# Optimization experiments

Measured on AMD Instinct MI355X. Metric: run time of the kernel, lower is better.

Reference implementation:

```python
import jax, jax.numpy as jnp
import numpy as np

N_NODES = 100000
N_EDGES = 1600000
D = 128
N_GRAPHS = 128
N_LAYERS = 3


def setup_inputs() -> dict:
    key = jax.random.key(0)
    ks = jax.random.split(key, 3 + 4 * N_LAYERS)
    x = jax.random.normal(ks[0], (N_NODES, D), dtype=jnp.float32)
    edge_index = jax.random.randint(ks[1], (2, N_EDGES), 0, N_NODES, dtype=jnp.int64)
    batch = jnp.sort(jax.random.randint(ks[2], (N_NODES,), 0, N_GRAPHS, dtype=jnp.int64))
    inp = {"x": x, "edge_index": edge_index, "batch": batch}
    scale = 1.0 / np.sqrt(D)
    for l in range(N_LAYERS):
        inp[f"W1_{l}"] = jax.random.normal(ks[3 + 4 * l], (D, D), dtype=jnp.float32) * scale
        inp[f"b1_{l}"] = jnp.zeros((D,), dtype=jnp.float32)
        inp[f"W2_{l}"] = jax.random.normal(ks[4 + 4 * l], (D, D), dtype=jnp.float32) * scale
        inp[f"b2_{l}"] = jnp.zeros((D,), dtype=jnp.float32)
    return inp


def _gin_conv(x, edge_index, W1, b1, W2, b2):
    # GINConv with eps=0: out = MLP(x + sum_{j in N(i)} x_j)
    msgs = x[edge_index[0]]                                   # [E, D] gather
    agg = jax.ops.segment_sum(msgs, edge_index[1], num_segments=N_NODES)
    h = x + agg
    h = jax.nn.relu(h @ W1 + b1)
    return h @ W2 + b2


def reference(x, edge_index, batch,
              W1_0, b1_0, W2_0, b2_0,
              W1_1, b1_1, W2_1, b2_1,
              W1_2, b1_2, W2_2, b2_2):
    params = [(W1_0, b1_0, W2_0, b2_0), (W1_1, b1_1, W2_1, b2_1), (W1_2, b1_2, W2_2, b2_2)]
    h = x
    for l in range(N_LAYERS - 1):
        h = _gin_conv(h, edge_index, *params[l])
        h = jax.nn.relu(h)  # act; dropout with drop_ratio=0 is identity
    node_emb = _gin_conv(h, edge_index, *params[-1])  # JK='last'
    # global_mean_pool
    sums = jax.ops.segment_sum(node_emb, batch, num_segments=N_GRAPHS)
    counts = jax.ops.segment_sum(jnp.ones((N_NODES, 1), node_emb.dtype), batch, num_segments=N_GRAPHS)
    graph_emb = sums / jnp.maximum(counts, 1.0)
    return graph_emb
```

## Files before the change

kernel.cpp:

```cpp
#include <hip/hip_runtime.h>
#include <hip/hip_bf16.h>

#define N_NODES 100000
#define N_PAD   100032
#define N_EDGES 1600000
#define DIM 128
#define N_GRAPHS 128
#define NBKT 98
#define BSTRIDE 18432
#define TILES (N_PAD / 16)
#define GRID_MLP 1024
#define POOL_BLKS ((N_NODES + 127) / 128)
#define B1_BATCH 4096
#define B1_GRID ((N_EDGES + B1_BATCH - 1) / B1_BATCH)

typedef unsigned short u16;
typedef unsigned int u32;
typedef __attribute__((ext_vector_type(8))) short bf16x8;
typedef __attribute__((ext_vector_type(4))) float f32x4;

#define MFMA(A, B, C) __builtin_amdgcn_mfma_f32_16x16x32_bf16(A, B, C, 0, 0, 0)

__device__ __forceinline__ u16 f2bf(float x) {
    u32 u = __float_as_uint(x);
    u = (u + 0x7FFFu + ((u >> 16) & 1u)) >> 16;
    return (u16)u;
}
__device__ __forceinline__ float bf2f(u16 u) {
    return __uint_as_float(((u32)u) << 16);
}

__global__ __launch_bounds__(256) void bucket1_kernel(const int* __restrict__ src,
                                                      const int* __restrict__ dst,
                                                      u32* __restrict__ cursorB,
                                                      u32* __restrict__ pairs) {
    __shared__ int lh[NBKT];
    __shared__ u32 lbase[NBKT];
    int t = threadIdx.x;
    if (t < NBKT) lh[t] = 0;
    __syncthreads();
    int e0 = blockIdx.x * B1_BATCH;
    int d[16], s[16], rk[16];
#pragma unroll
    for (int k = 0; k < 16; ++k) {
        int e = e0 + t + k * 256;
        if (e < N_EDGES) {
            d[k] = dst[e];
            s[k] = src[e];
            rk[k] = atomicAdd(&lh[d[k] >> 10], 1);
        }
    }
    __syncthreads();
    if (t < NBKT) lbase[t] = atomicAdd(&cursorB[t], (u32)lh[t]) + (u32)(t * BSTRIDE);
    __syncthreads();
#pragma unroll
    for (int k = 0; k < 16; ++k) {
        int e = e0 + t + k * 256;
        if (e < N_EDGES) {
            u32 pos = lbase[d[k] >> 10] + (u32)rk[k];
            pairs[pos] = ((u32)(d[k] & 1023) << 22) | (u32)s[k];
        }
    }
}

__global__ __launch_bounds__(1024) void bucket2_kernel(const u32* __restrict__ cursorB,
                                                       const u32* __restrict__ pairs,
                                                       int* __restrict__ row_ptr,
                                                       int* __restrict__ csr) {
    __shared__ int lh[1024];
    __shared__ int rc[1024];
    __shared__ int bs[128];
    int b = blockIdx.x, t = threadIdx.x;

    if (t < 128) bs[t] = (t < NBKT) ? (int)cursorB[t] : 0;
    __syncthreads();
    for (int off = 1; off < 128; off <<= 1) {
        int v = (t < 128 && t >= off) ? bs[t - off] : 0;
        __syncthreads();
        if (t < 128) bs[t] += v;
        __syncthreads();
    }
    int cnt = (int)cursorB[b];
    int bbase = (b == 0) ? 0 : bs[b - 1];

    lh[t] = 0;
    __syncthreads();
    const u32* pb = pairs + (size_t)b * BSTRIDE;
    for (int i = t; i < cnt; i += 1024) atomicAdd(&lh[__builtin_nontemporal_load(pb + i) >> 22], 1);
    __syncthreads();

    int own = lh[t];
    for (int off = 1; off < 1024; off <<= 1) {
        int v = (t >= off) ? lh[t - off] : 0;
        __syncthreads();
        lh[t] += v;
        __syncthreads();
    }
    int excl = lh[t] - own;
    int node = b * 1024 + t;
    if (node < N_NODES) row_ptr[node] = bbase + excl;
    if (b == 0 && t == 0) row_ptr[N_NODES] = N_EDGES;
    rc[t] = bbase + excl;
    __syncthreads();

    for (int i = t; i < cnt; i += 1024) {
        u32 p = __builtin_nontemporal_load(pb + i);
        int pos = atomicAdd(&rc[p >> 22], 1);
        csr[pos] = (int)(p & 0x3FFFFFu);
    }
}

__global__ __launch_bounds__(256) void xprep_kernel(const float* __restrict__ x,
                                                    u16* __restrict__ hb) {
    int i = blockIdx.x * 256 + threadIdx.x;
    if (i < N_NODES * 32) {
        float4 v = ((const float4*)x)[i];
        ushort4 o;
        o.x = f2bf(v.x); o.y = f2bf(v.y); o.z = f2bf(v.z); o.w = f2bf(v.w);
        ((ushort4*)hb)[i] = o;
    }
}

__global__ __launch_bounds__(256) void agg_kernel(const u16* __restrict__ hb,
                                                  const int* __restrict__ rp,
                                                  const int* __restrict__ csr,
                                                  u16* __restrict__ Ah) {
    int node = (blockIdx.x * 256 + threadIdx.x) >> 5;
    int l = threadIdx.x & 31;
    if (node >= N_NODES) return;
    const ushort4* h4 = (const ushort4*)hb;
    ushort4 sv = h4[(size_t)node * 32 + l];
    float a0 = bf2f(sv.x), a1 = bf2f(sv.y), a2 = bf2f(sv.z), a3 = bf2f(sv.w);
    int s = rp[node], e = rp[node + 1];
    int i = s;
    for (; i + 8 <= e; i += 8) {
        ushort4 v0 = h4[(size_t)csr[i + 0] * 32 + l];
        ushort4 v1 = h4[(size_t)csr[i + 1] * 32 + l];
        ushort4 v2 = h4[(size_t)csr[i + 2] * 32 + l];
        ushort4 v3 = h4[(size_t)csr[i + 3] * 32 + l];
        ushort4 v4 = h4[(size_t)csr[i + 4] * 32 + l];
        ushort4 v5 = h4[(size_t)csr[i + 5] * 32 + l];
        ushort4 v6 = h4[(size_t)csr[i + 6] * 32 + l];
        ushort4 v7 = h4[(size_t)csr[i + 7] * 32 + l];
        a0 += ((bf2f(v0.x) + bf2f(v1.x)) + (bf2f(v2.x) + bf2f(v3.x))) +
              ((bf2f(v4.x) + bf2f(v5.x)) + (bf2f(v6.x) + bf2f(v7.x)));
        a1 += ((bf2f(v0.y) + bf2f(v1.y)) + (bf2f(v2.y) + bf2f(v3.y))) +
              ((bf2f(v4.y) + bf2f(v5.y)) + (bf2f(v6.y) + bf2f(v7.y)));
        a2 += ((bf2f(v0.z) + bf2f(v1.z)) + (bf2f(v2.z) + bf2f(v3.z))) +
              ((bf2f(v4.z) + bf2f(v5.z)) + (bf2f(v6.z) + bf2f(v7.z)));
        a3 += ((bf2f(v0.w) + bf2f(v1.w)) + (bf2f(v2.w) + bf2f(v3.w))) +
              ((bf2f(v4.w) + bf2f(v5.w)) + (bf2f(v6.w) + bf2f(v7.w)));
    }
    for (; i < e; ++i) {
        ushort4 v = h4[(size_t)csr[i] * 32 + l];
        a0 += bf2f(v.x); a1 += bf2f(v.y); a2 += bf2f(v.z); a3 += bf2f(v.w);
    }
    ushort4 hv;
    hv.x = f2bf(a0); hv.y = f2bf(a1); hv.z = f2bf(a2); hv.w = f2bf(a3);
    *(ushort4*)(Ah + (size_t)node * 128 + l * 4) = hv;
}

struct WPrepArgs {
    const float* w[6];
    u16* buf[6];
};
__global__ __launch_bounds__(256) void wprep_kernel(WPrepArgs p) {
    int m = blockIdx.y;
    int idx = blockIdx.x * 256 + threadIdx.x;
    int n = idx >> 7, k = idx & 127;
    float v = p.w[m][k * 128 + n];
    u16 hi = f2bf(v);
    p.buf[m][idx] = hi;
    p.buf[m][idx + 16384] = f2bf(v - bf2f(hi));
}

#define HS 136
__global__ __launch_bounds__(256, 2) void fused_mlp(const u16* __restrict__ Ah,
                                                    const u16* __restrict__ W1,
                                                    const float* __restrict__ b1,
                                                    const u16* __restrict__ W2,
                                                    const float* __restrict__ b2,
                                                    float* __restrict__ Cf,
                                                    u16* __restrict__ Cb, int mode) {
    __shared__ u16 Hh[64 * HS];
    __shared__ u16 Hl[64 * HS];
    int tid = threadIdx.x;
    int lane = tid & 63, wave = tid >> 6;
    int m16 = lane & 15, quad = lane >> 4;
    int colBase = wave * 32;

    float b1v[2][4], b2v[2][4];
#pragma unroll
    for (int nt = 0; nt < 2; ++nt)
#pragma unroll
        for (int rg = 0; rg < 4; ++rg) {
            int col = colBase + nt * 16 + quad * 4 + rg;
            b1v[nt][rg] = b1[col];
            b2v[nt][rg] = b2[col];
        }

    f32x4 z = {0.f, 0.f, 0.f, 0.f};
    bf16x8 aH[4][4];

    int t0 = blockIdx.x * 4;
    if (t0 < TILES) {
#pragma unroll
        for (int p = 0; p < 4; ++p) {
            const u16* ah = Ah + (size_t)((t0 + p) * 16 + m16) * 128 + quad * 8;
#pragma unroll
            for (int kb = 0; kb < 4; ++kb)
                aH[p][kb] = *(const bf16x8*)(ah + kb * 32);
        }
    }

    for (; t0 < TILES; t0 += 4 * GRID_MLP) {
        bf16x8 W1H[2][4], W1L[2][4];
#pragma unroll
        for (int nt = 0; nt < 2; ++nt) {
            int n = colBase + nt * 16 + m16;
#pragma unroll
            for (int kb = 0; kb < 4; ++kb) {
                int off = n * 128 + kb * 32 + quad * 8;
                W1H[nt][kb] = *(const bf16x8*)(W1 + off);
                W1L[nt][kb] = *(const bf16x8*)(W1 + off + 16384);
            }
        }

        f32x4 acc[4][2];
#pragma unroll
        for (int p = 0; p < 4; ++p) { acc[p][0] = z; acc[p][1] = z; }

#pragma unroll
        for (int kb = 0; kb < 4; ++kb) {
#pragma unroll
            for (int p = 0; p < 4; ++p) {
                acc[p][0] = MFMA(W1H[0][kb], aH[p][kb], acc[p][0]);
                acc[p][1] = MFMA(W1H[1][kb], aH[p][kb], acc[p][1]);
                acc[p][0] = MFMA(W1L[0][kb], aH[p][kb], acc[p][0]);
                acc[p][1] = MFMA(W1L[1][kb], aH[p][kb], acc[p][1]);
            }
        }

        __syncthreads();

#pragma unroll
        for (int p = 0; p < 4; ++p) {
#pragma unroll
            for (int nt = 0; nt < 2; ++nt) {
                ushort4 hv, lv;
#pragma unroll
                for (int rg = 0; rg < 4; ++rg) {
                    float v = fmaxf(acc[p][nt][rg] + b1v[nt][rg], 0.f);
                    u16 hi = f2bf(v);
                    ((u16*)&hv)[rg] = hi;
                    ((u16*)&lv)[rg] = f2bf(v - bf2f(hi));
                }
                int off = (p * 16 + m16) * HS + colBase + nt * 16 + quad * 4;
                *(ushort4*)&Hh[off] = hv;
                *(ushort4*)&Hl[off] = lv;
            }
        }
        __syncthreads();

        int nt0 = t0 + 4 * GRID_MLP;
        if (nt0 < TILES) {
#pragma unroll
            for (int p = 0; p < 4; ++p) {
                const u16* ah = Ah + (size_t)((nt0 + p) * 16 + m16) * 128 + quad * 8;
#pragma unroll
                for (int kb = 0; kb < 4; ++kb)
                    aH[p][kb] = *(const bf16x8*)(ah + kb * 32);
            }
        }

        bf16x8 W2H[2][4], W2L[2][4];
#pragma unroll
        for (int nt = 0; nt < 2; ++nt) {
            int n = colBase + nt * 16 + m16;
#pragma unroll
            for (int kb = 0; kb < 4; ++kb) {
                int off = n * 128 + kb * 32 + quad * 8;
                W2H[nt][kb] = *(const bf16x8*)(W2 + off);
                W2L[nt][kb] = *(const bf16x8*)(W2 + off + 16384);
            }
        }

        f32x4 acc2[4][2];
#pragma unroll
        for (int p = 0; p < 4; ++p) { acc2[p][0] = z; acc2[p][1] = z; }
#pragma unroll
        for (int kb = 0; kb < 4; ++kb) {
#pragma unroll
            for (int p = 0; p < 4; ++p) {
                int off = (p * 16 + m16) * HS + kb * 32 + quad * 8;
                bf16x8 hH = *(const bf16x8*)(&Hh[off]);
                bf16x8 hL = *(const bf16x8*)(&Hl[off]);
                acc2[p][0] = MFMA(W2H[0][kb], hH, acc2[p][0]);
                acc2[p][1] = MFMA(W2H[1][kb], hH, acc2[p][1]);
                acc2[p][0] = MFMA(W2H[0][kb], hL, acc2[p][0]);
                acc2[p][1] = MFMA(W2H[1][kb], hL, acc2[p][1]);
                acc2[p][0] = MFMA(W2L[0][kb], hH, acc2[p][0]);
                acc2[p][1] = MFMA(W2L[1][kb], hH, acc2[p][1]);
            }
        }

#pragma unroll
        for (int p = 0; p < 4; ++p) {
            size_t row = (size_t)(t0 + p) * 16 + m16;
#pragma unroll
            for (int nt = 0; nt < 2; ++nt) {
                int col = colBase + nt * 16 + quad * 4;
                if (mode) {
                    ushort4 o;
#pragma unroll
                    for (int rg = 0; rg < 4; ++rg)
                        ((u16*)&o)[rg] = f2bf(fmaxf(acc2[p][nt][rg] + b2v[nt][rg], 0.f));
                    *(ushort4*)(Cb + row * 128 + col) = o;
                } else {
                    float4 o;
                    o.x = acc2[p][nt][0] + b2v[nt][0];
                    o.y = acc2[p][nt][1] + b2v[nt][1];
                    o.z = acc2[p][nt][2] + b2v[nt][2];
                    o.w = acc2[p][nt][3] + b2v[nt][3];
                    *(float4*)(Cf + row * 128 + col) = o;
                }
            }
        }
    }
}

__global__ __launch_bounds__(256) void psum_kernel(const float* __restrict__ h,
                                                   const int* __restrict__ batch,
                                                   float* __restrict__ sums) {
    __shared__ int sBatch[128];
    int blk = blockIdx.x, t = threadIdx.x;
    int n0 = blk * 128;
    int nEnd = min(n0 + 128, N_NODES);
    if (t < 128 && n0 + t < N_NODES) sBatch[t] = batch[n0 + t];
    __syncthreads();

    int j = t & 127;
    int half = t >> 7;
    int s = n0 + half * 64;
    int e = min(s + 64, nEnd);

    float acc = 0.f;
    int cur = -1;
    for (int n = s; n < e; ++n) {
        int g = sBatch[n - n0];
        if (g != cur) {
            if (cur >= 0) atomicAdd(&sums[cur * 128 + j], acc);
            cur = g;
            acc = 0.f;
        }
        acc += h[(size_t)n * 128 + j];
    }
    if (cur >= 0) atomicAdd(&sums[cur * 128 + j], acc);
}

__global__ __launch_bounds__(128) void pdiv_kernel(const float* __restrict__ sums,
                                                   const int* __restrict__ batch,
                                                   float* __restrict__ out) {
    __shared__ int sB[2];
    int g = blockIdx.x;
    if (threadIdx.x < 2) {
        int target = g + threadIdx.x;
        int lo = 0, hi = N_NODES;
        while (lo < hi) {
            int m = (lo + hi) >> 1;
            if (batch[m] < target) lo = m + 1; else hi = m;
        }
        sB[threadIdx.x] = lo;
    }
    __syncthreads();
    float cnt = (float)(sB[1] - sB[0]);
    out[g * 128 + threadIdx.x] = sums[g * 128 + threadIdx.x] / fmaxf(cnt, 1.f);
}

extern "C" void kernel_launch(void* const* d_in, const int* in_sizes, int n_in,
                              void* d_out, int out_size, void* d_ws, size_t ws_size,
                              hipStream_t stream) {
    const float* x     = (const float*)d_in[0];
    const int*   ei    = (const int*)d_in[1];
    const int*   batch = (const int*)d_in[2];
    const int*   eSrc  = ei;
    const int*   eDst  = ei + N_EDGES;

    const float* W1[3] = {(const float*)d_in[3], (const float*)d_in[7],  (const float*)d_in[11]};
    const float* b1[3] = {(const float*)d_in[4], (const float*)d_in[8],  (const float*)d_in[12]};
    const float* W2[3] = {(const float*)d_in[5], (const float*)d_in[9],  (const float*)d_in[13]};
    const float* b2[3] = {(const float*)d_in[6], (const float*)d_in[10], (const float*)d_in[14]};

    float* P2 = (float*)d_ws;
    u16*   hb = (u16*)(P2 + (size_t)N_PAD * DIM);
    u16*   Ah = hb + (size_t)N_PAD * DIM;
    u16*   Wb = Ah + (size_t)N_PAD * DIM;
    int*   row_ptr = (int*)(Wb + 6 * 32768);
    u32*   cursorB = (u32*)(row_ptr + N_NODES + 8);
    int*   csr     = (int*)(cursorB + 128);
    float* sums    = (float*)(csr + N_EDGES);
    u32*   pairs   = (u32*)P2;

    hipMemsetAsync(cursorB, 0, 128 * sizeof(u32), stream);
    bucket1_kernel<<<B1_GRID, 256, 0, stream>>>(eSrc, eDst, cursorB, pairs);
    bucket2_kernel<<<NBKT, 1024, 0, stream>>>(cursorB, pairs, row_ptr, csr);

    xprep_kernel<<<(N_NODES * 32 + 255) / 256, 256, 0, stream>>>(x, hb);
    WPrepArgs wp;
    for (int l = 0; l < 3; ++l) {
        wp.w[2 * l]       = W1[l];
        wp.w[2 * l + 1]   = W2[l];
        wp.buf[2 * l]     = Wb + (size_t)(2 * l) * 32768;
        wp.buf[2 * l + 1] = Wb + (size_t)(2 * l + 1) * 32768;
    }
    wprep_kernel<<<dim3(64, 6), 256, 0, stream>>>(wp);
    hipMemsetAsync(sums, 0, N_GRAPHS * DIM * sizeof(float), stream);

    const int aggGrid = (N_NODES * 32 + 255) / 256;

    for (int l = 0; l < 3; ++l) {
        agg_kernel<<<aggGrid, 256, 0, stream>>>(hb, row_ptr, csr, Ah);
        fused_mlp<<<GRID_MLP, 256, 0, stream>>>(Ah,
                                                Wb + (size_t)(2 * l) * 32768, b1[l],
                                                Wb + (size_t)(2 * l + 1) * 32768, b2[l],
                                                P2, hb, (l < 2) ? 1 : 0);
    }
    psum_kernel<<<POOL_BLKS, 256, 0, stream>>>(P2, batch, sums);
    pdiv_kernel<<<N_GRAPHS, 128, 0, stream>>>(sums, batch, (float*)d_out);
}
```

Baseline: 510.6 us.

## Use one tile-group per MLP block and store final layer output as bf16

The fused MLP kernel drops its grid-stride loop and cross-iteration prefetch, and launches enough blocks (1563) for each to handle a single 64-row tile group. The last layer now writes bf16 into the shared hb buffer instead of a separate fp32 array, and the pooling kernel reads bf16, roughly halving the bytes moved by that store and by pooling. In exchange, final node embeddings are rounded to bf16 before the mean pool, which adds some error, and each block reloads the weights.

```diff
diff --git a/kernel.cpp b/kernel.cpp
--- a/kernel.cpp
+++ b/kernel.cpp
@@ -9,7 +9,7 @@
 #define NBKT 98
 #define BSTRIDE 18432
 #define TILES (N_PAD / 16)
-#define GRID_MLP 1024
+#define GRID_MLP 1563
 #define POOL_BLKS ((N_NODES + 127) / 128)
 #define B1_BATCH 4096
 #define B1_GRID ((N_EDGES + B1_BATCH - 1) / B1_BATCH)
@@ -180,8 +180,7 @@
                                                     const float* __restrict__ b1,
                                                     const u16* __restrict__ W2,
                                                     const float* __restrict__ b2,
-                                                    float* __restrict__ Cf,
-                                                    u16* __restrict__ Cb, int mode) {
+                                                    u16* __restrict__ Cb, int relu) {
     __shared__ u16 Hh[64 * HS];
     __shared__ u16 Hl[64 * HS];
     int tid = threadIdx.x;
@@ -203,133 +202,111 @@
     bf16x8 aH[4][4];
 
     int t0 = blockIdx.x * 4;
-    if (t0 < TILES) {
+    if (t0 >= TILES) return;
+#pragma unroll
+    for (int p = 0; p < 4; ++p) {
+        const u16* ah = Ah + (size_t)((t0 + p) * 16 + m16) * 128 + quad * 8;
+#pragma unroll
+        for (int kb = 0; kb < 4; ++kb)
+            aH[p][kb] = *(const bf16x8*)(ah + kb * 32);
+    }
+
+    bf16x8 W1H[2][4], W1L[2][4];
+#pragma unroll
+    for (int nt = 0; nt < 2; ++nt) {
+        int n = colBase + nt * 16 + m16;
+#pragma unroll
+        for (int kb = 0; kb < 4; ++kb) {
+            int off = n * 128 + kb * 32 + quad * 8;
+            W1H[nt][kb] = *(const bf16x8*)(W1 + off);
+            W1L[nt][kb] = *(const bf16x8*)(W1 + off + 16384);
+        }
+    }
+
+    f32x4 acc[4][2];
+#pragma unroll
+    for (int p = 0; p < 4; ++p) { acc[p][0] = z; acc[p][1] = z; }
+
+#pragma unroll
+    for (int kb = 0; kb < 4; ++kb) {
 #pragma unroll
         for (int p = 0; p < 4; ++p) {
-            const u16* ah = Ah + (size_t)((t0 + p) * 16 + m16) * 128 + quad * 8;
-#pragma unroll
-            for (int kb = 0; kb < 4; ++kb)
-                aH[p][kb] = *(const bf16x8*)(ah + kb * 32);
-        }
-    }
-
-    for (; t0 < TILES; t0 += 4 * GRID_MLP) {
-        bf16x8 W1H[2][4], W1L[2][4];
+            acc[p][0] = MFMA(W1H[0][kb], aH[p][kb], acc[p][0]);
+            acc[p][1] = MFMA(W1H[1][kb], aH[p][kb], acc[p][1]);
+            acc[p][0] = MFMA(W1L[0][kb], aH[p][kb], acc[p][0]);
+            acc[p][1] = MFMA(W1L[1][kb], aH[p][kb], acc[p][1]);
+        }
+    }
+
+#pragma unroll
+    for (int p = 0; p < 4; ++p) {
 #pragma unroll
         for (int nt = 0; nt < 2; ++nt) {
-            int n = colBase + nt * 16 + m16;
-#pragma unroll
-            for (int kb = 0; kb < 4; ++kb) {
-                int off = n * 128 + kb * 32 + quad * 8;
-                W1H[nt][kb] = *(const bf16x8*)(W1 + off);
-                W1L[nt][kb] = *(const bf16x8*)(W1 + off + 16384);
+            ushort4 hv, lv;
+#pragma unroll
+            for (int rg = 0; rg < 4; ++rg) {
+                float v = fmaxf(acc[p][nt][rg] + b1v[nt][rg], 0.f);
+                u16 hi = f2bf(v);
+                ((u16*)&hv)[rg] = hi;
+                ((u16*)&lv)[rg] = f2bf(v - bf2f(hi));
             }
-        }
-
-        f32x4 acc[4][2];
-#pragma unroll
-        for (int p = 0; p < 4; ++p) { acc[p][0] = z; acc[p][1] = z; }
-
+            int off = (p * 16 + m16) * HS + colBase + nt * 16 + quad * 4;
+            *(ushort4*)&Hh[off] = hv;
+            *(ushort4*)&Hl[off] = lv;
+        }
+    }
+    __syncthreads();
+
+    bf16x8 W2H[2][4], W2L[2][4];
+#pragma unroll
+    for (int nt = 0; nt < 2; ++nt) {
+        int n = colBase + nt * 16 + m16;
 #pragma unroll
         for (int kb = 0; kb < 4; ++kb) {
-#pragma unroll
-            for (int p = 0; p < 4; ++p) {
-                acc[p][0] = MFMA(W1H[0][kb], aH[p][kb], acc[p][0]);
-                acc[p][1] = MFMA(W1H[1][kb], aH[p][kb], acc[p][1]);
-                acc[p][0] = MFMA(W1L[0][kb], aH[p][kb], acc[p][0]);
-                acc[p][1] = MFMA(W1L[1][kb], aH[p][kb], acc[p][1]);
+            int off = n * 128 + kb * 32 + quad * 8;
+            W2H[nt][kb] = *(const bf16x8*)(W2 + off);
+            W2L[nt][kb] = *(const bf16x8*)(W2 + off + 16384);
+        }
+    }
+
+    f32x4 acc2[4][2];
+#pragma unroll
+    for (int p = 0; p < 4; ++p) { acc2[p][0] = z; acc2[p][1] = z; }
+#pragma unroll
+    for (int kb = 0; kb < 4; ++kb) {
+#pragma unroll
+        for (int p = 0; p < 4; ++p) {
+            int off = (p * 16 + m16) * HS + kb * 32 + quad * 8;
+            bf16x8 hH = *(const bf16x8*)(&Hh[off]);
+            bf16x8 hL = *(const bf16x8*)(&Hl[off]);
+            acc2[p][0] = MFMA(W2H[0][kb], hH, acc2[p][0]);
+            acc2[p][1] = MFMA(W2H[1][kb], hH, acc2[p][1]);
+            acc2[p][0] = MFMA(W2H[0][kb], hL, acc2[p][0]);
+            acc2[p][1] = MFMA(W2H[1][kb], hL, acc2[p][1]);
+            acc2[p][0] = MFMA(W2L[0][kb], hH, acc2[p][0]);
+            acc2[p][1] = MFMA(W2L[1][kb], hH, acc2[p][1]);
+        }
+    }
+
+#pragma unroll
+    for (int p = 0; p < 4; ++p) {
+        size_t row = (size_t)(t0 + p) * 16 + m16;
+#pragma unroll
+        for (int nt = 0; nt < 2; ++nt) {
+            int col = colBase + nt * 16 + quad * 4;
+            ushort4 o;
+#pragma unroll
+            for (int rg = 0; rg < 4; ++rg) {
+                float v = acc2[p][nt][rg] + b2v[nt][rg];
+                if (relu) v = fmaxf(v, 0.f);
+                ((u16*)&o)[rg] = f2bf(v);
             }
-        }
-
-        __syncthreads();
-
-#pragma unroll
-        for (int p = 0; p < 4; ++p) {
-#pragma unroll
-            for (int nt = 0; nt < 2; ++nt) {
-                ushort4 hv, lv;
-#pragma unroll
-                for (int rg = 0; rg < 4; ++rg) {
-                    float v = fmaxf(acc[p][nt][rg] + b1v[nt][rg], 0.f);
-                    u16 hi = f2bf(v);
-                    ((u16*)&hv)[rg] = hi;
-                    ((u16*)&lv)[rg] = f2bf(v - bf2f(hi));
-                }
-                int off = (p * 16 + m16) * HS + colBase + nt * 16 + quad * 4;
-                *(ushort4*)&Hh[off] = hv;
-                *(ushort4*)&Hl[off] = lv;
-            }
-        }
-        __syncthreads();
-
-        int nt0 = t0 + 4 * GRID_MLP;
-        if (nt0 < TILES) {
-#pragma unroll
-            for (int p = 0; p < 4; ++p) {
-                const u16* ah = Ah + (size_t)((nt0 + p) * 16 + m16) * 128 + quad * 8;
-#pragma unroll
-                for (int kb = 0; kb < 4; ++kb)
-                    aH[p][kb] = *(const bf16x8*)(ah + kb * 32);
-            }
-        }
-
-        bf16x8 W2H[2][4], W2L[2][4];
-#pragma unroll
-        for (int nt = 0; nt < 2; ++nt) {
-            int n = colBase + nt * 16 + m16;
-#pragma unroll
-            for (int kb = 0; kb < 4; ++kb) {
-                int off = n * 128 + kb * 32 + quad * 8;
-                W2H[nt][kb] = *(const bf16x8*)(W2 + off);
-                W2L[nt][kb] = *(const bf16x8*)(W2 + off + 16384);
-            }
-        }
-
-        f32x4 acc2[4][2];
-#pragma unroll
-        for (int p = 0; p < 4; ++p) { acc2[p][0] = z; acc2[p][1] = z; }
-#pragma unroll
-        for (int kb = 0; kb < 4; ++kb) {
-#pragma unroll
-            for (int p = 0; p < 4; ++p) {
-                int off = (p * 16 + m16) * HS + kb * 32 + quad * 8;
-                bf16x8 hH = *(const bf16x8*)(&Hh[off]);
-                bf16x8 hL = *(const bf16x8*)(&Hl[off]);
-                acc2[p][0] = MFMA(W2H[0][kb], hH, acc2[p][0]);
-                acc2[p][1] = MFMA(W2H[1][kb], hH, acc2[p][1]);
-                acc2[p][0] = MFMA(W2H[0][kb], hL, acc2[p][0]);
-                acc2[p][1] = MFMA(W2H[1][kb], hL, acc2[p][1]);
-                acc2[p][0] = MFMA(W2L[0][kb], hH, acc2[p][0]);
-                acc2[p][1] = MFMA(W2L[1][kb], hH, acc2[p][1]);
-            }
-        }
-
-#pragma unroll
-        for (int p = 0; p < 4; ++p) {
-            size_t row = (size_t)(t0 + p) * 16 + m16;
-#pragma unroll
-            for (int nt = 0; nt < 2; ++nt) {
-                int col = colBase + nt * 16 + quad * 4;
-                if (mode) {
-                    ushort4 o;
-#pragma unroll
-                    for (int rg = 0; rg < 4; ++rg)
-                        ((u16*)&o)[rg] = f2bf(fmaxf(acc2[p][nt][rg] + b2v[nt][rg], 0.f));
-                    *(ushort4*)(Cb + row * 128 + col) = o;
-                } else {
-                    float4 o;
-                    o.x = acc2[p][nt][0] + b2v[nt][0];
-                    o.y = acc2[p][nt][1] + b2v[nt][1];
-                    o.z = acc2[p][nt][2] + b2v[nt][2];
-                    o.w = acc2[p][nt][3] + b2v[nt][3];
-                    *(float4*)(Cf + row * 128 + col) = o;
-                }
-            }
-        }
-    }
-}
-
-__global__ __launch_bounds__(256) void psum_kernel(const float* __restrict__ h,
+            *(ushort4*)(Cb + row * 128 + col) = o;
+        }
+    }
+}
+
+__global__ __launch_bounds__(256) void psum_kernel(const u16* __restrict__ h,
                                                    const int* __restrict__ batch,
                                                    float* __restrict__ sums) {
     __shared__ int sBatch[128];
@@ -353,7 +330,7 @@
             cur = g;
             acc = 0.f;
         }
-        acc += h[(size_t)n * 128 + j];
+        acc += bf2f(h[(size_t)n * 128 + j]);
     }
     if (cur >= 0) atomicAdd(&sums[cur * 128 + j], acc);
 }
@@ -423,8 +400,8 @@
         fused_mlp<<<GRID_MLP, 256, 0, stream>>>(Ah,
                                                 Wb + (size_t)(2 * l) * 32768, b1[l],
                                                 Wb + (size_t)(2 * l + 1) * 32768, b2[l],
-                                                P2, hb, (l < 2) ? 1 : 0);
-    }
-    psum_kernel<<<POOL_BLKS, 256, 0, stream>>>(P2, batch, sums);
+                                                hb, (l < 2) ? 1 : 0);
+    }
+    psum_kernel<<<POOL_BLKS, 256, 0, stream>>>(hb, batch, sums);
     pdiv_kernel<<<N_GRAPHS, 128, 0, stream>>>(sums, batch, (float*)d_out);
 }
```

New measurement: 519.3 us. No clear change (+1.7%).
